# Performance work log

Hardware: AMD Instinct MI355X
Metric: run time of the kernel (lower is better)

## Reference

```python
import jax, jax.numpy as jnp
import numpy as np

N, D, K = 8192, 2048, 256
# amnesic weights at train iteration 0: _i = 2 < n1 = 20 -> l = 0
W1 = 0.5  # (_i - 1 - l) / _i
W2 = 0.5  # (1 + l) / _i


def setup_inputs() -> dict:
    key = jax.random.key(0)
    k1, k2 = jax.random.split(key)
    x = jax.random.normal(k1, (N, D), dtype=jnp.float32)
    V0 = 0.1 * jax.random.normal(k2, (D, K), dtype=jnp.float32)  # init eigen vectors
    return {"x": x, "V0": V0}


def reference(x, V0):
    # x: [N, D] input batch; V0: [D, K] unnormalized eigenvector estimates (_v)
    d0 = jnp.linalg.norm(V0, axis=0)  # per-column norms, as in init_eigen_vectors setter

    def step(r, inp):
        v, d = inp  # v: [D] current unnormalized component, d: scalar norm
        # CCIPCA update: v' = w1*v + w2 * r^T (r v) / d
        u = W1 * v + (W2 / d) * (r.T @ (r @ v))
        dn = jnp.linalg.norm(u)
        vn = u / dn
        # deflate residual: r <- r - (r vn) vn^T
        r = r - jnp.outer(r @ vn, vn)
        return r, vn

    _, vns = jax.lax.scan(step, x, (V0.T, d0))  # vns: [K, D] normalized components
    # project original input on updated components: x.mm(self.v)
    return x @ vns.T  # [N, K]
```

## Files before the change

### kernel.cpp

```cpp
#include <hip/hip_runtime.h>
#include <math.h>

#define NN 8192
#define DD 2048
#define KK 256
#define NB 256
#define RPB 8
#define NGRP 16
#define GSZ 16

__device__ __forceinline__ float blockReduceSum(float val, float* sdata) {
    for (int off = 32; off > 0; off >>= 1)
        val += __shfl_down(val, off, 64);
    int wid = threadIdx.x >> 6;
    int lane = threadIdx.x & 63;
    __syncthreads();
    if (lane == 0) sdata[wid] = val;
    __syncthreads();
    return sdata[0] + sdata[1] + sdata[2] + sdata[3];
}

__device__ __forceinline__ float agload(const float* p) {
    return __hip_atomic_load(p, __ATOMIC_RELAXED, __HIP_MEMORY_SCOPE_AGENT);
}
__device__ __forceinline__ void agstore(float* p, float v) {
    __hip_atomic_store(p, v, __ATOMIC_RELAXED, __HIP_MEMORY_SCOPE_AGENT);
}

__device__ __forceinline__ void dfsync(unsigned* grpc, unsigned* rootc, int slot, int b) {
    if (threadIdx.x == 0) {
        asm volatile("s_waitcnt vmcnt(0)" ::: "memory");
        int grp = b >> 4;
        unsigned* gw = grpc + ((size_t)slot * NGRP + grp) * 16;
        unsigned* rw = rootc + (size_t)slot * 16;
        unsigned prev = __hip_atomic_fetch_add(gw, 1u, __ATOMIC_RELAXED, __HIP_MEMORY_SCOPE_AGENT);
        if (prev == GSZ - 1u)
            __hip_atomic_fetch_add(rw, 1u, __ATOMIC_RELAXED, __HIP_MEMORY_SCOPE_AGENT);
        while (__hip_atomic_load(rw, __ATOMIC_RELAXED, __HIP_MEMORY_SCOPE_AGENT) < (unsigned)NGRP)
            __builtin_amdgcn_s_sleep(2);
    }
    __syncthreads();
}

__global__ void ktranspose(const float* __restrict__ V0, float* __restrict__ V0T) {
    __shared__ float tile[32][33];
    int bx = blockIdx.x;
    int by = blockIdx.y;
    int tx = threadIdx.x % 32;
    int ty = threadIdx.x / 32;
    for (int r = ty; r < 32; r += 8)
        tile[r][tx] = V0[(size_t)(bx * 32 + r) * KK + by * 32 + tx];
    __syncthreads();
    for (int r = ty; r < 32; r += 8)
        V0T[(size_t)(by * 32 + r) * DD + bx * 32 + tx] = tile[tx][r];
}

__global__ void kd0(const float* __restrict__ V0T, float* __restrict__ d0) {
    __shared__ float sdata[4];
    int k = blockIdx.x;
    float acc = 0.f;
    for (int j = threadIdx.x; j < DD; j += 256) {
        float v = V0T[(size_t)k * DD + j];
        acc += v * v;
    }
    float s = blockReduceSum(acc, sdata);
    if (threadIdx.x == 0) d0[k] = sqrtf(s);
}

__global__ void ksyrk(const float* __restrict__ x, float* __restrict__ G) {
    __shared__ float As[32][68];
    __shared__ float Bs[32][68];
    int t = blockIdx.x;
    int bj = (int)((sqrtf(8.0f * (float)t + 1.0f) - 1.0f) * 0.5f);
    while ((bj + 1) * (bj + 2) / 2 <= t) ++bj;
    while (bj * (bj + 1) / 2 > t) --bj;
    int bi = t - bj * (bj + 1) / 2;
    int a0 = bi * 64, b0 = bj * 64;
    int tid = threadIdx.x;
    int al = tid % 64;
    int nl0 = tid / 64;
    int tr = tid / 16, tc = tid % 16;
    float acc[4][4] = {};
    for (int n0 = 0; n0 < NN; n0 += 32) {
        for (int pass = 0; pass < 8; ++pass) {
            int nl = nl0 + pass * 4;
            As[nl][al] = x[(size_t)(n0 + nl) * DD + a0 + al];
            Bs[nl][al] = x[(size_t)(n0 + nl) * DD + b0 + al];
        }
        __syncthreads();
        for (int kk2 = 0; kk2 < 32; ++kk2) {
            float4 a4 = *(const float4*)&As[kk2][tr * 4];
            float4 b4 = *(const float4*)&Bs[kk2][tc * 4];
            float a[4] = {a4.x, a4.y, a4.z, a4.w};
            float b[4] = {b4.x, b4.y, b4.z, b4.w};
            for (int i = 0; i < 4; ++i)
                for (int j = 0; j < 4; ++j)
                    acc[i][j] += a[i] * b[j];
        }
        __syncthreads();
    }
    for (int i = 0; i < 4; ++i) {
        float4 o = make_float4(acc[i][0], acc[i][1], acc[i][2], acc[i][3]);
        *(float4*)&G[(size_t)(a0 + tr * 4 + i) * DD + b0 + tc * 4] = o;
    }
    if (bi != bj) {
        for (int i = 0; i < 4; ++i)
            for (int j = 0; j < 4; ++j)
                G[(size_t)(b0 + tc * 4 + j) * DD + a0 + tr * 4 + i] = acc[i][j];
    }
}

__global__ void kmatvecG(const float* __restrict__ G, const float* __restrict__ v,
                         float* __restrict__ s) {
    __shared__ float vs[DD];
    int tid = threadIdx.x;
    for (int t2 = 0; t2 < 8; ++t2) vs[tid + t2 * 256] = v[tid + t2 * 256];
    __syncthreads();
    int wave = tid >> 6, lane = tid & 63;
    int row = blockIdx.x * 4 + wave;
    const float* Gr = G + (size_t)row * DD;
    float a = 0.f;
    for (int c = 0; c < 8; ++c) {
        int idx = lane * 4 + c * 256;
        float4 gq = *(const float4*)(Gr + idx);
        float4 vq = *(const float4*)(vs + idx);
        a += gq.x * vq.x + gq.y * vq.y + gq.z * vq.z + gq.w * vq.w;
    }
    for (int off = 32; off > 0; off >>= 1) a += __shfl_down(a, off, 64);
    if (lane == 0) s[row] = a;
}

__global__ void kstep1(const float* __restrict__ G, const float* __restrict__ V0T,
                       const float* __restrict__ d0, const float* __restrict__ s,
                       float* __restrict__ g, float* __restrict__ Vn, int k) {
    __shared__ float u[DD];
    __shared__ float sdata[4];
    __shared__ float sinv;
    int tid = threadIdx.x;
    const float* v = V0T + (size_t)k * DD;
    float cf = 0.5f / d0[k];
    float acc = 0.f;
    for (int t2 = 0; t2 < 8; ++t2) {
        int j = tid + t2 * 256;
        float uj = 0.5f * v[j] + cf * s[j];
        u[j] = uj;
        acc += uj * uj;
    }
    float n2 = blockReduceSum(acc, sdata);
    if (tid == 0) sinv = 1.0f / sqrtf(n2);
    __syncthreads();
    float inv = sinv;
    if (blockIdx.x == 0) {
        for (int t2 = 0; t2 < 8; ++t2) {
            int j = tid + t2 * 256;
            Vn[(size_t)k * DD + j] = u[j] * inv;
        }
    }
    int wave = tid >> 6, lane = tid & 63;
    int row = blockIdx.x * 4 + wave;
    const float* Gr = G + (size_t)row * DD;
    float a = 0.f;
    for (int c = 0; c < 8; ++c) {
        int idx = lane * 4 + c * 256;
        float4 gq = *(const float4*)(Gr + idx);
        float4 uq = *(const float4*)(u + idx);
        a += gq.x * uq.x + gq.y * uq.y + gq.z * uq.z + gq.w * uq.w;
    }
    for (int off = 32; off > 0; off >>= 1) a += __shfl_down(a, off, 64);
    if (lane == 0) g[row] = a * inv;
}

__global__ void kstep2(float* __restrict__ G, const float* __restrict__ V0T,
                       const float* __restrict__ Vn, const float* __restrict__ g,
                       float* __restrict__ s_next, int k, int knext) {
    __shared__ float vn_s[DD];
    __shared__ float h_s[DD];
    __shared__ float w_s[DD];
    __shared__ float sdata[4];
    int tid = threadIdx.x;
    float acc = 0.f;
    for (int t2 = 0; t2 < 8; ++t2) {
        int j = tid + t2 * 256;
        float vnj = Vn[(size_t)k * DD + j];
        float gj = g[j];
        vn_s[j] = vnj;
        h_s[j] = gj;
        w_s[j] = V0T[(size_t)knext * DD + j];
        acc += vnj * gj;
    }
    float c = blockReduceSum(acc, sdata);
    for (int t2 = 0; t2 < 8; ++t2) {
        int j = tid + t2 * 256;
        h_s[j] -= c * vn_s[j];
    }
    __syncthreads();
    int wave = tid >> 6, lane = tid & 63;
    int row = blockIdx.x * 4 + wave;
    float vni = vn_s[row], gi = g[row];
    float* Gr = G + (size_t)row * DD;
    float a = 0.f;
    for (int cc = 0; cc < 8; ++cc) {
        int idx = lane * 4 + cc * 256;
        float4 Gq = *(float4*)(Gr + idx);
        float4 hq = *(const float4*)(h_s + idx);
        float4 vq = *(const float4*)(vn_s + idx);
        float4 wq = *(const float4*)(w_s + idx);
        Gq.x = Gq.x - vni * hq.x - gi * vq.x;
        Gq.y = Gq.y - vni * hq.y - gi * vq.y;
        Gq.z = Gq.z - vni * hq.z - gi * vq.z;
        Gq.w = Gq.w - vni * hq.w - gi * vq.w;
        a += Gq.x * wq.x + Gq.y * wq.y + Gq.z * wq.z + Gq.w * wq.w;
        *(float4*)(Gr + idx) = Gq;
    }
    for (int off = 32; off > 0; off >>= 1) a += __shfl_down(a, off, 64);
    if (lane == 0) s_next[row] = a;
}

__global__ void __launch_bounds__(1024, 4) kloop5(
    float* __restrict__ G, const float* __restrict__ V0T,
    const float* __restrict__ d0v, float* __restrict__ Vn,
    float* __restrict__ gbuf, float* __restrict__ wbuf,
    float* __restrict__ accbuf, unsigned* rootc, unsigned* grpc) {
    __shared__ float vbuf[2][DD];
    __shared__ float gs[DD];
    __shared__ float vx[DD];
    __shared__ float scal[8];
    __shared__ float partg[16], partw[16];

    const int tid = threadIdx.x;
    const int b = blockIdx.x;
    const int wave = tid >> 6, lane = tid & 63;
    const int rowi = wave >> 1;
    const int half = wave & 1;
    const int row = b * RPB + rowi;
    const int d0i = tid, d1i = tid + 1024;
    const int ib = half * 1024 + lane * 4;
    const float* Gr = G + (size_t)row * DD;

    float4 Gq[4];
    #pragma unroll
    for (int c = 0; c < 4; ++c) Gq[c] = *(const float4*)(Gr + ib + c * 256);

    vbuf[0][d0i] = 0.f;
    vbuf[0][d1i] = 0.f;
    vx[d0i] = V0T[d0i];
    vx[d1i] = V0T[d1i];
    __syncthreads();
    {
        float aw = 0.f;
        #pragma unroll
        for (int c = 0; c < 4; ++c) {
            float4 xq = *(const float4*)(vx + ib + c * 256);
            aw += Gq[c].x * xq.x + Gq[c].y * xq.y + Gq[c].z * xq.z + Gq[c].w * xq.w;
        }
        for (int off = 32; off > 0; off >>= 1) aw += __shfl_down(aw, off, 64);
        if (lane == 0) partw[wave] = aw;
    }
    __syncthreads();
    if (tid < RPB) {
        int rg = b * RPB + tid;
        agstore(&wbuf[rg], partw[2 * tid] + partw[2 * tid + 1]);
    }
    if (tid < 8) {
        float sacc = 0.f;
        for (int r = 0; r < RPB; ++r) {
            int rg = b * RPB + r;
            float wr = partw[2 * r] + partw[2 * r + 1];
            if (tid == 3) sacc += wr * wr;
            else if (tid == 6) sacc += wr * vx[rg];
        }
        agstore(&accbuf[(size_t)tid * NB + b], sacc);
    }
    dfsync(grpc, rootc, 0, b);

    for (int k = 0; k < KK; ++k) {
        const int p = k & 1;
        const float* vnp = vbuf[p];
        float* vnew = vbuf[p ^ 1];
        const float* gsrc = gbuf + (size_t)p * DD;
        const float* wsrc = wbuf + (size_t)p * DD;
        float* gdst = gbuf + (size_t)(p ^ 1) * DD;
        float* wdst = wbuf + (size_t)(p ^ 1) * DD;
        const float* vk = V0T + (size_t)k * DD;

        if (wave < 8) {
            const float* ap = accbuf + (size_t)k * (8 * NB) + (size_t)wave * NB + lane * 4;
            float sp = agload(ap) + agload(ap + 1) + agload(ap + 2) + agload(ap + 3);
            for (int off = 32; off > 0; off >>= 1) sp += __shfl_down(sp, off, 64);
            if (lane == 0) scal[wave] = sp;
        }
        float g0 = agload(&gsrc[d0i]), g1 = agload(&gsrc[d1i]);
        float w0 = agload(&wsrc[d0i]), w1 = agload(&wsrc[d1i]);
        float vk0 = vk[d0i], vk1 = vk[d1i];
        float vp0 = vnp[d0i], vp1 = vnp[d1i];
        __syncthreads();

        float A1 = scal[0], A2 = scal[1], A3 = scal[2], A4 = scal[3];
        float A5 = scal[4], A6 = scal[5], A7 = scal[6], A8 = scal[7];
        float d0k = d0v[k];
        float cf = 0.5f / d0k;
        float c_s = A1;
        float alpha = A2 - A1 * A3;
        float beta = A3;
        float ss = A4 + alpha * alpha + beta * beta * A8
                 - 2.f * alpha * A6 - 2.f * beta * A5 + 2.f * alpha * beta * A1;
        float vks = A7 - alpha * A3 - beta * A2;
        float n2 = 0.25f * d0k * d0k + cf * vks + cf * cf * ss;
        float inv = 1.0f / sqrtf(n2);

        gs[d0i] = g0;
        gs[d1i] = g1;
        float u0 = 0.5f * vk0 + cf * (w0 - alpha * vp0 - beta * g0);
        float u1 = 0.5f * vk1 + cf * (w1 - alpha * vp1 - beta * g1);
        vnew[d0i] = u0 * inv;
        vnew[d1i] = u1 * inv;
        if (k < KK - 1) {
            vx[d0i] = V0T[(size_t)(k + 1) * DD + d0i];
            vx[d1i] = V0T[(size_t)(k + 1) * DD + d1i];
        }
        __syncthreads();

        if (tid < RPB) {
            int rg = b * RPB + tid;
            agstore(&Vn[(size_t)k * DD + rg], vnew[rg]);
        }
        if (k == KK - 1) break;

        {
            float a_r = vnp[row];
            float g_r = gs[row];
            float b_r = g_r - c_s * a_r;
            float ag = 0.f, aw = 0.f;
            #pragma unroll
            for (int c = 0; c < 4; ++c) {
                int idx = ib + c * 256;
                float4 gq = *(const float4*)(gs + idx);
                float4 vq = *(const float4*)(vnp + idx);
                float4 nq = *(const float4*)(vnew + idx);
                float4 xq = *(const float4*)(vx + idx);
                Gq[c].x -= a_r * gq.x + b_r * vq.x;
                Gq[c].y -= a_r * gq.y + b_r * vq.y;
                Gq[c].z -= a_r * gq.z + b_r * vq.z;
                Gq[c].w -= a_r * gq.w + b_r * vq.w;
                ag += Gq[c].x * nq.x + Gq[c].y * nq.y + Gq[c].z * nq.z + Gq[c].w * nq.w;
                aw += Gq[c].x * xq.x + Gq[c].y * xq.y + Gq[c].z * xq.z + Gq[c].w * xq.w;
            }
            for (int off = 32; off > 0; off >>= 1) {
                ag += __shfl_down(ag, off, 64);
                aw += __shfl_down(aw, off, 64);
            }
            if (lane == 0) { partg[wave] = ag; partw[wave] = aw; }
        }
        __syncthreads();
        if (tid < RPB) {
            int rg = b * RPB + tid;
            agstore(&gdst[rg], partg[2 * tid] + partg[2 * tid + 1]);
            agstore(&wdst[rg], partw[2 * tid] + partw[2 * tid + 1]);
        }
        if (tid < 8) {
            float sacc = 0.f;
            for (int r = 0; r < RPB; ++r) {
                int rg = b * RPB + r;
                float gr = partg[2 * r] + partg[2 * r + 1];
                float wr = partw[2 * r] + partw[2 * r + 1];
                float vnr = vnew[rg];
                float vxr = vx[rg];
                float t;
                switch (tid) {
                    case 0: t = vnr * gr; break;
                    case 1: t = gr * vxr; break;
                    case 2: t = vnr * vxr; break;
                    case 3: t = wr * wr; break;
                    case 4: t = wr * gr; break;
                    case 5: t = wr * vnr; break;
                    case 6: t = wr * vxr; break;
                    default: t = gr * gr; break;
                }
                sacc += t;
            }
            agstore(&accbuf[(size_t)(k + 1) * (8 * NB) + (size_t)tid * NB + b], sacc);
        }
        dfsync(grpc, rootc, k + 1, b);
    }
}

__global__ void kout(const float* __restrict__ x, const float* __restrict__ Vn,
                     float* __restrict__ out) {
    __shared__ float As[32][68];
    __shared__ float Bs[32][68];
    int i0 = blockIdx.x * 64;
    int k0 = blockIdx.y * 64;
    int tid = threadIdx.x;
    int tr = tid / 16;
    int tc = tid % 16;
    float acc[4][4] = {};
    for (int j0 = 0; j0 < DD; j0 += 32) {
        int c = tid % 32;
        int r0 = tid / 32;
        for (int pass = 0; pass < 8; ++pass) {
            int rr = r0 + pass * 8;
            As[c][rr] = x[(size_t)(i0 + rr) * DD + j0 + c];
            Bs[c][rr] = Vn[(size_t)(k0 + rr) * DD + j0 + c];
        }
        __syncthreads();
        for (int kk = 0; kk < 32; ++kk) {
            float4 a4 = *(const float4*)&As[kk][tr * 4];
            float4 b4 = *(const float4*)&Bs[kk][tc * 4];
            float a[4] = {a4.x, a4.y, a4.z, a4.w};
            float b[4] = {b4.x, b4.y, b4.z, b4.w};
            for (int ar = 0; ar < 4; ++ar)
                for (int bc = 0; bc < 4; ++bc)
                    acc[ar][bc] += a[ar] * b[bc];
        }
        __syncthreads();
    }
    for (int ar = 0; ar < 4; ++ar) {
        float4 o = make_float4(acc[ar][0], acc[ar][1], acc[ar][2], acc[ar][3]);
        *(float4*)&out[(size_t)(i0 + tr * 4 + ar) * KK + k0 + tc * 4] = o;
    }
}

extern "C" void kernel_launch(void* const* d_in, const int* in_sizes, int n_in,
                              void* d_out, int out_size, void* d_ws, size_t ws_size,
                              hipStream_t stream) {
    const float* x  = (const float*)d_in[0];
    const float* V0 = (const float*)d_in[1];
    float* out = (float*)d_out;

    float* G    = (float*)d_ws;
    float* V0T  = G + (size_t)DD * DD;
    float* Vn   = V0T + (size_t)KK * DD;
    float* gbuf = Vn + (size_t)KK * DD;
    float* wbuf = gbuf + 2 * DD;
    float* d0   = wbuf + 2 * DD;
    float* accbuf = d0 + KK;
    unsigned* rootc = (unsigned*)(accbuf + (size_t)KK * 8 * NB);
    unsigned* grpc  = rootc + (size_t)KK * 16;

    ktranspose<<<dim3(DD / 32, KK / 32), 256, 0, stream>>>(V0, V0T);
    kd0<<<KK, 256, 0, stream>>>(V0T, d0);
    ksyrk<<<528, 256, 0, stream>>>(x, G);

    hipMemsetAsync(rootc, 0, ((size_t)KK * 16 + (size_t)KK * NGRP * 16) * sizeof(unsigned), stream);
    hipMemsetAsync(gbuf, 0, DD * sizeof(float), stream);

    void* kargs[] = {(void*)&G, (void*)&V0T, (void*)&d0, (void*)&Vn,
                     (void*)&gbuf, (void*)&wbuf, (void*)&accbuf,
                     (void*)&rootc, (void*)&grpc};
    hipError_t cerr = hipLaunchCooperativeKernel(kloop5, dim3(NB), dim3(1024),
                                                 kargs, 0, stream);
    if (cerr != hipSuccess) {
        float* g = gbuf;
        float* sbuf = wbuf;
        kmatvecG<<<512, 256, 0, stream>>>(G, V0T, sbuf);
        for (int k = 0; k < KK; ++k) {
            float* s_cur = sbuf + (k & 1) * DD;
            float* s_nxt = sbuf + ((k + 1) & 1) * DD;
            kstep1<<<512, 256, 0, stream>>>(G, V0T, d0, s_cur, g, Vn, k);
            if (k < KK - 1)
                kstep2<<<512, 256, 0, stream>>>(G, V0T, Vn, g, s_nxt, k, k + 1);
        }
    }

    kout<<<dim3(NN / 64, KK / 64), 256, 0, stream>>>(x, Vn, out);
}
```

Before: 3.270 ms.

## Replace per-step grid barrier with poison-flag dataflow waits on per-step buffers

Removes the hierarchical atomic-counter grid barrier that ran after every one of the 256 steps. Each block now spins only until the eight partial-sum slots it needs for step k no longer hold a 0xFFFFFFFF poison pattern. The g and w vectors become per-step buffers, so no double-buffer slot is overwritten while another block still reads it, and their loads move after the wait. The poison pattern costs extra memsets of the per-step buffers. Correctness relies on relaxed agent-scope stores being ordered by an s_waitcnt in wave 0, which is a memory-ordering risk.

```diff
diff --git a/kernel.cpp b/kernel.cpp
--- a/kernel.cpp
+++ b/kernel.cpp
@@ -6,8 +6,7 @@
 #define KK 256
 #define NB 256
 #define RPB 8
-#define NGRP 16
-#define GSZ 16
+#define POISON 0xFFFFFFFFu
 
 __device__ __forceinline__ float blockReduceSum(float val, float* sdata) {
     for (int off = 32; off > 0; off >>= 1)
@@ -26,20 +25,8 @@
 __device__ __forceinline__ void agstore(float* p, float v) {
     __hip_atomic_store(p, v, __ATOMIC_RELAXED, __HIP_MEMORY_SCOPE_AGENT);
 }
-
-__device__ __forceinline__ void dfsync(unsigned* grpc, unsigned* rootc, int slot, int b) {
-    if (threadIdx.x == 0) {
-        asm volatile("s_waitcnt vmcnt(0)" ::: "memory");
-        int grp = b >> 4;
-        unsigned* gw = grpc + ((size_t)slot * NGRP + grp) * 16;
-        unsigned* rw = rootc + (size_t)slot * 16;
-        unsigned prev = __hip_atomic_fetch_add(gw, 1u, __ATOMIC_RELAXED, __HIP_MEMORY_SCOPE_AGENT);
-        if (prev == GSZ - 1u)
-            __hip_atomic_fetch_add(rw, 1u, __ATOMIC_RELAXED, __HIP_MEMORY_SCOPE_AGENT);
-        while (__hip_atomic_load(rw, __ATOMIC_RELAXED, __HIP_MEMORY_SCOPE_AGENT) < (unsigned)NGRP)
-            __builtin_amdgcn_s_sleep(2);
-    }
-    __syncthreads();
+__device__ __forceinline__ unsigned agloadu(const unsigned* p) {
+    return __hip_atomic_load(p, __ATOMIC_RELAXED, __HIP_MEMORY_SCOPE_AGENT);
 }
 
 __global__ void ktranspose(const float* __restrict__ V0, float* __restrict__ V0T) {
@@ -216,11 +203,11 @@
     if (lane == 0) s_next[row] = a;
 }
 
-__global__ void __launch_bounds__(1024, 4) kloop5(
+__global__ void __launch_bounds__(1024, 4) kloop6(
     float* __restrict__ G, const float* __restrict__ V0T,
     const float* __restrict__ d0v, float* __restrict__ Vn,
-    float* __restrict__ gbuf, float* __restrict__ wbuf,
-    float* __restrict__ accbuf, unsigned* rootc, unsigned* grpc) {
+    float* __restrict__ gbufK, float* __restrict__ wbufK,
+    float* __restrict__ accbuf) {
     __shared__ float vbuf[2][DD];
     __shared__ float gs[DD];
     __shared__ float vx[DD];
@@ -259,8 +246,10 @@
     __syncthreads();
     if (tid < RPB) {
         int rg = b * RPB + tid;
-        agstore(&wbuf[rg], partw[2 * tid] + partw[2 * tid + 1]);
-    }
+        agstore(&wbufK[rg], partw[2 * tid] + partw[2 * tid + 1]);
+        agstore(&gbufK[rg], 0.f);
+    }
+    if (wave == 0) asm volatile("s_waitcnt vmcnt(0)" ::: "memory");
     if (tid < 8) {
         float sacc = 0.f;
         for (int r = 0; r < RPB; ++r) {
@@ -271,28 +260,31 @@
         }
         agstore(&accbuf[(size_t)tid * NB + b], sacc);
     }
-    dfsync(grpc, rootc, 0, b);
 
     for (int k = 0; k < KK; ++k) {
         const int p = k & 1;
         const float* vnp = vbuf[p];
         float* vnew = vbuf[p ^ 1];
-        const float* gsrc = gbuf + (size_t)p * DD;
-        const float* wsrc = wbuf + (size_t)p * DD;
-        float* gdst = gbuf + (size_t)(p ^ 1) * DD;
-        float* wdst = wbuf + (size_t)(p ^ 1) * DD;
+        const float* gsrc = gbufK + (size_t)k * DD;
+        const float* wsrc = wbufK + (size_t)k * DD;
         const float* vk = V0T + (size_t)k * DD;
 
         if (wave < 8) {
-            const float* ap = accbuf + (size_t)k * (8 * NB) + (size_t)wave * NB + lane * 4;
-            float sp = agload(ap) + agload(ap + 1) + agload(ap + 2) + agload(ap + 3);
+            const unsigned* ap = (const unsigned*)accbuf
+                                 + (size_t)k * (8 * NB) + (size_t)wave * NB + lane * 4;
+            unsigned x0, x1, x2, x3;
+            for (;;) {
+                x0 = agloadu(ap); x1 = agloadu(ap + 1);
+                x2 = agloadu(ap + 2); x3 = agloadu(ap + 3);
+                bool bad = (x0 == POISON) | (x1 == POISON) | (x2 == POISON) | (x3 == POISON);
+                if (!__any(bad)) break;
+                __builtin_amdgcn_s_sleep(1);
+            }
+            float sp = __uint_as_float(x0) + __uint_as_float(x1)
+                     + __uint_as_float(x2) + __uint_as_float(x3);
             for (int off = 32; off > 0; off >>= 1) sp += __shfl_down(sp, off, 64);
             if (lane == 0) scal[wave] = sp;
         }
-        float g0 = agload(&gsrc[d0i]), g1 = agload(&gsrc[d1i]);
-        float w0 = agload(&wsrc[d0i]), w1 = agload(&wsrc[d1i]);
-        float vk0 = vk[d0i], vk1 = vk[d1i];
-        float vp0 = vnp[d0i], vp1 = vnp[d1i];
         __syncthreads();
 
         float A1 = scal[0], A2 = scal[1], A3 = scal[2], A4 = scal[3];
@@ -308,6 +300,10 @@
         float n2 = 0.25f * d0k * d0k + cf * vks + cf * cf * ss;
         float inv = 1.0f / sqrtf(n2);
 
+        float g0 = agload(&gsrc[d0i]), g1 = agload(&gsrc[d1i]);
+        float w0 = agload(&wsrc[d0i]), w1 = agload(&wsrc[d1i]);
+        float vk0 = vk[d0i], vk1 = vk[d1i];
+        float vp0 = vnp[d0i], vp1 = vnp[d1i];
         gs[d0i] = g0;
         gs[d1i] = g1;
         float u0 = 0.5f * vk0 + cf * (w0 - alpha * vp0 - beta * g0);
@@ -354,9 +350,10 @@
         __syncthreads();
         if (tid < RPB) {
             int rg = b * RPB + tid;
-            agstore(&gdst[rg], partg[2 * tid] + partg[2 * tid + 1]);
-            agstore(&wdst[rg], partw[2 * tid] + partw[2 * tid + 1]);
-        }
+            agstore(&gbufK[(size_t)(k + 1) * DD + rg], partg[2 * tid] + partg[2 * tid + 1]);
+            agstore(&wbufK[(size_t)(k + 1) * DD + rg], partw[2 * tid] + partw[2 * tid + 1]);
+        }
+        if (wave == 0) asm volatile("s_waitcnt vmcnt(0)" ::: "memory");
         if (tid < 8) {
             float sacc = 0.f;
             for (int r = 0; r < RPB; ++r) {
@@ -380,7 +377,6 @@
             }
             agstore(&accbuf[(size_t)(k + 1) * (8 * NB) + (size_t)tid * NB + b], sacc);
         }
-        dfsync(grpc, rootc, k + 1, b);
     }
 }
 
@@ -427,31 +423,29 @@
     const float* V0 = (const float*)d_in[1];
     float* out = (float*)d_out;
 
-    float* G    = (float*)d_ws;
-    float* V0T  = G + (size_t)DD * DD;
-    float* Vn   = V0T + (size_t)KK * DD;
-    float* gbuf = Vn + (size_t)KK * DD;
-    float* wbuf = gbuf + 2 * DD;
-    float* d0   = wbuf + 2 * DD;
-    float* accbuf = d0 + KK;
-    unsigned* rootc = (unsigned*)(accbuf + (size_t)KK * 8 * NB);
-    unsigned* grpc  = rootc + (size_t)KK * 16;
+    float* G     = (float*)d_ws;
+    float* V0T   = G + (size_t)DD * DD;
+    float* Vn    = V0T + (size_t)KK * DD;
+    float* gbufK = Vn + (size_t)KK * DD;
+    float* wbufK = gbufK + (size_t)KK * DD;
+    float* accbuf = wbufK + (size_t)KK * DD;
+    float* d0    = accbuf + (size_t)KK * 8 * NB;
 
     ktranspose<<<dim3(DD / 32, KK / 32), 256, 0, stream>>>(V0, V0T);
     kd0<<<KK, 256, 0, stream>>>(V0T, d0);
     ksyrk<<<528, 256, 0, stream>>>(x, G);
 
-    hipMemsetAsync(rootc, 0, ((size_t)KK * 16 + (size_t)KK * NGRP * 16) * sizeof(unsigned), stream);
-    hipMemsetAsync(gbuf, 0, DD * sizeof(float), stream);
+    hipMemsetAsync(gbufK, 0xFF, (size_t)KK * DD * sizeof(float), stream);
+    hipMemsetAsync(wbufK, 0xFF, (size_t)KK * DD * sizeof(float), stream);
+    hipMemsetAsync(accbuf, 0xFF, (size_t)KK * 8 * NB * sizeof(float), stream);
 
     void* kargs[] = {(void*)&G, (void*)&V0T, (void*)&d0, (void*)&Vn,
-                     (void*)&gbuf, (void*)&wbuf, (void*)&accbuf,
-                     (void*)&rootc, (void*)&grpc};
-    hipError_t cerr = hipLaunchCooperativeKernel(kloop5, dim3(NB), dim3(1024),
+                     (void*)&gbufK, (void*)&wbufK, (void*)&accbuf};
+    hipError_t cerr = hipLaunchCooperativeKernel(kloop6, dim3(NB), dim3(1024),
                                                  kargs, 0, stream);
     if (cerr != hipSuccess) {
-        float* g = gbuf;
-        float* sbuf = wbuf;
+        float* g = gbufK;
+        float* sbuf = wbufK;
         kmatvecG<<<512, 256, 0, stream>>>(G, V0T, sbuf);
         for (int k = 0; k < KK; ++k) {
             float* s_cur = sbuf + (k & 1) * DD;
```

Measured after the change: 3.857 ms. 17.9% more time.

## Use 128x128 SYRK tiles and compute per-step scalars block-locally instead of via global partials

Applied to the files above, without the earlier changes.

The Gram-matrix SYRK kernel moves from 64x64 tiles with 4x4 per-thread accumulators to 128x128 tiles with 8x8 accumulators and vectorised float4 loads. This raises arithmetic intensity and cuts the block count to 136. In the persistent cooperative loop, the eight per-block partial scalar sums written to a global accumulation buffer are removed. Each block now recomputes the needed dot products and the norm directly from the full shared g/w/v vectors, using intra-block reductions. This trades extra redundant per-block work and two extra barriers per step for less global traffic and less serial tail work per iteration.

```diff
diff --git a/kernel.cpp b/kernel.cpp
--- a/kernel.cpp
+++ b/kernel.cpp
@@ -67,46 +67,60 @@
     if (threadIdx.x == 0) d0[k] = sqrtf(s);
 }
 
-__global__ void ksyrk(const float* __restrict__ x, float* __restrict__ G) {
-    __shared__ float As[32][68];
-    __shared__ float Bs[32][68];
+__global__ void ksyrk128(const float* __restrict__ x, float* __restrict__ G) {
+    __shared__ float As[16][132];
+    __shared__ float Bs[16][132];
     int t = blockIdx.x;
     int bj = (int)((sqrtf(8.0f * (float)t + 1.0f) - 1.0f) * 0.5f);
     while ((bj + 1) * (bj + 2) / 2 <= t) ++bj;
     while (bj * (bj + 1) / 2 > t) --bj;
     int bi = t - bj * (bj + 1) / 2;
-    int a0 = bi * 64, b0 = bj * 64;
+    int a0 = bi * 128, b0 = bj * 128;
     int tid = threadIdx.x;
-    int al = tid % 64;
-    int nl0 = tid / 64;
-    int tr = tid / 16, tc = tid % 16;
-    float acc[4][4] = {};
-    for (int n0 = 0; n0 < NN; n0 += 32) {
-        for (int pass = 0; pass < 8; ++pass) {
-            int nl = nl0 + pass * 4;
-            As[nl][al] = x[(size_t)(n0 + nl) * DD + a0 + al];
-            Bs[nl][al] = x[(size_t)(n0 + nl) * DD + b0 + al];
-        }
-        __syncthreads();
-        for (int kk2 = 0; kk2 < 32; ++kk2) {
-            float4 a4 = *(const float4*)&As[kk2][tr * 4];
-            float4 b4 = *(const float4*)&Bs[kk2][tc * 4];
-            float a[4] = {a4.x, a4.y, a4.z, a4.w};
-            float b[4] = {b4.x, b4.y, b4.z, b4.w};
-            for (int i = 0; i < 4; ++i)
-                for (int j = 0; j < 4; ++j)
-                    acc[i][j] += a[i] * b[j];
-        }
-        __syncthreads();
-    }
-    for (int i = 0; i < 4; ++i) {
-        float4 o = make_float4(acc[i][0], acc[i][1], acc[i][2], acc[i][3]);
-        *(float4*)&G[(size_t)(a0 + tr * 4 + i) * DD + b0 + tc * 4] = o;
+    int ldr = tid >> 5;
+    int ldc = (tid & 31) * 4;
+    int tr = tid >> 4, tc = tid & 15;
+    float acc[8][8] = {};
+    for (int n0 = 0; n0 < NN; n0 += 16) {
+        *(float4*)&As[ldr][ldc]     = *(const float4*)&x[(size_t)(n0 + ldr) * DD + a0 + ldc];
+        *(float4*)&As[ldr + 8][ldc] = *(const float4*)&x[(size_t)(n0 + ldr + 8) * DD + a0 + ldc];
+        *(float4*)&Bs[ldr][ldc]     = *(const float4*)&x[(size_t)(n0 + ldr) * DD + b0 + ldc];
+        *(float4*)&Bs[ldr + 8][ldc] = *(const float4*)&x[(size_t)(n0 + ldr + 8) * DD + b0 + ldc];
+        __syncthreads();
+        for (int kk = 0; kk < 16; ++kk) {
+            float4 alo = *(const float4*)&As[kk][tr * 4];
+            float4 ahi = *(const float4*)&As[kk][64 + tr * 4];
+            float4 blo = *(const float4*)&Bs[kk][tc * 4];
+            float4 bhi = *(const float4*)&Bs[kk][64 + tc * 4];
+            float a[8] = {alo.x, alo.y, alo.z, alo.w, ahi.x, ahi.y, ahi.z, ahi.w};
+            float bb[8] = {blo.x, blo.y, blo.z, blo.w, bhi.x, bhi.y, bhi.z, bhi.w};
+            #pragma unroll
+            for (int i = 0; i < 8; ++i)
+                #pragma unroll
+                for (int j = 0; j < 8; ++j)
+                    acc[i][j] += a[i] * bb[j];
+        }
+        __syncthreads();
+    }
+    #pragma unroll
+    for (int i = 0; i < 8; ++i) {
+        int lr = (i < 4) ? (tr * 4 + i) : (64 + tr * 4 + i - 4);
+        size_t gr = (size_t)(a0 + lr) * DD;
+        *(float4*)&G[gr + b0 + tc * 4] =
+            make_float4(acc[i][0], acc[i][1], acc[i][2], acc[i][3]);
+        *(float4*)&G[gr + b0 + 64 + tc * 4] =
+            make_float4(acc[i][4], acc[i][5], acc[i][6], acc[i][7]);
     }
     if (bi != bj) {
-        for (int i = 0; i < 4; ++i)
-            for (int j = 0; j < 4; ++j)
-                G[(size_t)(b0 + tc * 4 + j) * DD + a0 + tr * 4 + i] = acc[i][j];
+        #pragma unroll
+        for (int i = 0; i < 8; ++i) {
+            int lr = (i < 4) ? (tr * 4 + i) : (64 + tr * 4 + i - 4);
+            #pragma unroll
+            for (int j = 0; j < 8; ++j) {
+                int lc = (j < 4) ? (tc * 4 + j) : (64 + tc * 4 + j - 4);
+                G[(size_t)(b0 + lc) * DD + a0 + lr] = acc[i][j];
+            }
+        }
     }
 }
 
@@ -216,15 +230,16 @@
     if (lane == 0) s_next[row] = a;
 }
 
-__global__ void __launch_bounds__(1024, 4) kloop5(
+__global__ void __launch_bounds__(1024, 4) kloop7(
     float* __restrict__ G, const float* __restrict__ V0T,
     const float* __restrict__ d0v, float* __restrict__ Vn,
     float* __restrict__ gbuf, float* __restrict__ wbuf,
-    float* __restrict__ accbuf, unsigned* rootc, unsigned* grpc) {
+    unsigned* rootc, unsigned* grpc) {
     __shared__ float vbuf[2][DD];
     __shared__ float gs[DD];
     __shared__ float vx[DD];
-    __shared__ float scal[8];
+    __shared__ float red[3][16];
+    __shared__ float redN[16];
     __shared__ float partg[16], partw[16];
 
     const int tid = threadIdx.x;
@@ -260,16 +275,7 @@
     if (tid < RPB) {
         int rg = b * RPB + tid;
         agstore(&wbuf[rg], partw[2 * tid] + partw[2 * tid + 1]);
-    }
-    if (tid < 8) {
-        float sacc = 0.f;
-        for (int r = 0; r < RPB; ++r) {
-            int rg = b * RPB + r;
-            float wr = partw[2 * r] + partw[2 * r + 1];
-            if (tid == 3) sacc += wr * wr;
-            else if (tid == 6) sacc += wr * vx[rg];
-        }
-        agstore(&accbuf[(size_t)tid * NB + b], sacc);
+        agstore(&gbuf[rg], 0.f);
     }
     dfsync(grpc, rootc, 0, b);
 
@@ -283,35 +289,39 @@
         float* wdst = wbuf + (size_t)(p ^ 1) * DD;
         const float* vk = V0T + (size_t)k * DD;
 
-        if (wave < 8) {
-            const float* ap = accbuf + (size_t)k * (8 * NB) + (size_t)wave * NB + lane * 4;
-            float sp = agload(ap) + agload(ap + 1) + agload(ap + 2) + agload(ap + 3);
-            for (int off = 32; off > 0; off >>= 1) sp += __shfl_down(sp, off, 64);
-            if (lane == 0) scal[wave] = sp;
-        }
         float g0 = agload(&gsrc[d0i]), g1 = agload(&gsrc[d1i]);
         float w0 = agload(&wsrc[d0i]), w1 = agload(&wsrc[d1i]);
         float vk0 = vk[d0i], vk1 = vk[d1i];
         float vp0 = vnp[d0i], vp1 = vnp[d1i];
-        __syncthreads();
-
-        float A1 = scal[0], A2 = scal[1], A3 = scal[2], A4 = scal[3];
-        float A5 = scal[4], A6 = scal[5], A7 = scal[6], A8 = scal[7];
-        float d0k = d0v[k];
-        float cf = 0.5f / d0k;
-        float c_s = A1;
-        float alpha = A2 - A1 * A3;
-        float beta = A3;
-        float ss = A4 + alpha * alpha + beta * beta * A8
-                 - 2.f * alpha * A6 - 2.f * beta * A5 + 2.f * alpha * beta * A1;
-        float vks = A7 - alpha * A3 - beta * A2;
-        float n2 = 0.25f * d0k * d0k + cf * vks + cf * cf * ss;
-        float inv = 1.0f / sqrtf(n2);
-
         gs[d0i] = g0;
         gs[d1i] = g1;
+        float pc = vp0 * g0 + vp1 * g1;
+        float pgv = g0 * vk0 + g1 * vk1;
+        float pbv = vp0 * vk0 + vp1 * vk1;
+        for (int off = 32; off > 0; off >>= 1) {
+            pc += __shfl_down(pc, off, 64);
+            pgv += __shfl_down(pgv, off, 64);
+            pbv += __shfl_down(pbv, off, 64);
+        }
+        if (lane == 0) { red[0][wave] = pc; red[1][wave] = pgv; red[2][wave] = pbv; }
+        __syncthreads();
+        float c_s = 0.f, gv = 0.f, bv = 0.f;
+        #pragma unroll
+        for (int i = 0; i < 16; ++i) { c_s += red[0][i]; gv += red[1][i]; bv += red[2][i]; }
+        float alpha = gv - c_s * bv;
+        float beta = bv;
+        float cf = 0.5f / d0v[k];
+
         float u0 = 0.5f * vk0 + cf * (w0 - alpha * vp0 - beta * g0);
         float u1 = 0.5f * vk1 + cf * (w1 - alpha * vp1 - beta * g1);
+        float pn = u0 * u0 + u1 * u1;
+        for (int off = 32; off > 0; off >>= 1) pn += __shfl_down(pn, off, 64);
+        if (lane == 0) redN[wave] = pn;
+        __syncthreads();
+        float n2 = 0.f;
+        #pragma unroll
+        for (int i = 0; i < 16; ++i) n2 += redN[i];
+        float inv = 1.0f / sqrtf(n2);
         vnew[d0i] = u0 * inv;
         vnew[d1i] = u1 * inv;
         if (k < KK - 1) {
@@ -357,29 +367,6 @@
             agstore(&gdst[rg], partg[2 * tid] + partg[2 * tid + 1]);
             agstore(&wdst[rg], partw[2 * tid] + partw[2 * tid + 1]);
         }
-        if (tid < 8) {
-            float sacc = 0.f;
-            for (int r = 0; r < RPB; ++r) {
-                int rg = b * RPB + r;
-                float gr = partg[2 * r] + partg[2 * r + 1];
-                float wr = partw[2 * r] + partw[2 * r + 1];
-                float vnr = vnew[rg];
-                float vxr = vx[rg];
-                float t;
-                switch (tid) {
-                    case 0: t = vnr * gr; break;
-                    case 1: t = gr * vxr; break;
-                    case 2: t = vnr * vxr; break;
-                    case 3: t = wr * wr; break;
-                    case 4: t = wr * gr; break;
-                    case 5: t = wr * vnr; break;
-                    case 6: t = wr * vxr; break;
-                    default: t = gr * gr; break;
-                }
-                sacc += t;
-            }
-            agstore(&accbuf[(size_t)(k + 1) * (8 * NB) + (size_t)tid * NB + b], sacc);
-        }
         dfsync(grpc, rootc, k + 1, b);
     }
 }
@@ -433,21 +420,18 @@
     float* gbuf = Vn + (size_t)KK * DD;
     float* wbuf = gbuf + 2 * DD;
     float* d0   = wbuf + 2 * DD;
-    float* accbuf = d0 + KK;
-    unsigned* rootc = (unsigned*)(accbuf + (size_t)KK * 8 * NB);
+    unsigned* rootc = (unsigned*)(d0 + KK);
     unsigned* grpc  = rootc + (size_t)KK * 16;
 
     ktranspose<<<dim3(DD / 32, KK / 32), 256, 0, stream>>>(V0, V0T);
     kd0<<<KK, 256, 0, stream>>>(V0T, d0);
-    ksyrk<<<528, 256, 0, stream>>>(x, G);
+    ksyrk128<<<136, 256, 0, stream>>>(x, G);
 
     hipMemsetAsync(rootc, 0, ((size_t)KK * 16 + (size_t)KK * NGRP * 16) * sizeof(unsigned), stream);
-    hipMemsetAsync(gbuf, 0, DD * sizeof(float), stream);
 
     void* kargs[] = {(void*)&G, (void*)&V0T, (void*)&d0, (void*)&Vn,
-                     (void*)&gbuf, (void*)&wbuf, (void*)&accbuf,
-                     (void*)&rootc, (void*)&grpc};
-    hipError_t cerr = hipLaunchCooperativeKernel(kloop5, dim3(NB), dim3(1024),
+                     (void*)&gbuf, (void*)&wbuf, (void*)&rootc, (void*)&grpc};
+    hipError_t cerr = hipLaunchCooperativeKernel(kloop7, dim3(NB), dim3(1024),
                                                  kargs, 0, stream);
     if (cerr != hipSuccess) {
         float* g = gbuf;
```

Result: faster. 2.952 ms (-9.7%).
